# Kernel tuning notes

Measured on AMD Instinct MI355X. Metric: run time of the kernel, lower is better.

Reference implementation:

```python
import math
import jax
import jax.numpy as jnp
from jax import lax
import numpy as np

B, T, S, C, E = 16, 1024, 2048, 256, 256
STRIDE, MAX_SAMPLES, SIGMA, RAND_START = 20, 20, 3.0, 0


def setup_inputs():
    key = jax.random.key(0)
    ks = jax.random.split(key, 6)
    return {
        "x": jax.random.normal(ks[0], (B, T, C), jnp.float32),
        "target_embedding": jax.random.normal(ks[1], (B, T, E), jnp.float32),
        # scale keys so pre-softmax scores are O(1..10) like a trained model
        "enc_keys": jax.random.normal(ks[2], (B, E, S), jnp.float32) * 0.05,
        "enc_values": jax.random.normal(ks[3], (B, S, E), jnp.float32),
        "W_in": jax.random.normal(ks[4], (E, C), jnp.float32) * math.sqrt(1.0 / C),
        "b_in": jnp.zeros((E,), jnp.float32),
        "W_out": jax.random.normal(ks[5], (C, E), jnp.float32) * math.sqrt(1.0 / E),
        "b_out": jnp.zeros((C,), jnp.float32),
    }


def _get_matrix(attn, sim_vec, stride, start):
    # attn: [B,T,S], sim_vec: [B,S,E]
    nrm = sim_vec / jnp.linalg.norm(sim_vec, axis=2, keepdims=True)
    attn_avg = jnp.mean(attn, axis=1)[..., None]          # [B,S,1]
    ns = nrm[:, start::stride, :]                          # [B,N,E]
    aa = attn_avg[:, start::stride, :]                     # [B,N,1]
    sim = jnp.einsum('bne,bme->bnm', ns, ns)               # cosine similarity
    qual = aa @ jnp.swapaxes(aa, 1, 2)                     # quality outer product
    return qual * sim                                      # DPP kernel L [B,N,N]


def _bfgm(L, max_samples):
    # Vectorized faithful version of the greedy Cholesky DPP MAP loop.
    Bv, N, _ = L.shape
    bidx = jnp.arange(Bv)
    D0 = jnp.diagonal(L, axis1=1, axis2=2)                 # [B,N]
    mask0 = jnp.ones((Bv, N), L.dtype)
    J0 = jnp.argmax(jnp.log(D0 * mask0), axis=1)
    mask0 = mask0.at[bidx, J0].set(0.0)
    C0 = jnp.zeros((Bv, N, max_samples), L.dtype)          # col 0 stays zero (as in torch)

    def step(carry, t):
        Cm, D, J, mask = carry
        Lj = L[bidx, J, :]                                 # [B,N] = L[b, J[b], i]
        cj = Cm[bidx, J, :]                                # [B,K]
        cdot = jnp.einsum('bnk,bk->bn', Cm, cj)            # <c_i, c_j>
        dj = D[bidx, J][:, None]
        e = (Lj - cdot) / dj * mask                        # zero at already-selected
        Cm = Cm.at[:, :, t].set(e)
        D = D - e * e
        J = jnp.argmax(jnp.log(D * mask), axis=1)
        mask = mask.at[bidx, J].set(0.0)
        return (Cm, D, J, mask), J

    (_, _, _, _), Js = lax.scan(step, (C0, D0, J0, mask0), jnp.arange(1, max_samples))
    all_J = jnp.concatenate([J0[None, :], Js], axis=0).T   # [B,max_samples]
    return jnp.sort(all_J, axis=1)                         # = nonzero(1-mask) order


def _create_gm(mu, sigma, length):
    pos = jnp.arange(length, dtype=jnp.float32)            # [S]
    z = pos[None, None, :] - mu[:, :, None].astype(jnp.float32)
    g = jnp.exp(-(z * z) / (2.0 * sigma * sigma)) / (math.sqrt(2.0 * math.pi) * sigma)
    return jnp.sum(g, axis=1)                              # [B,S]


def _forward(x, target_embedding, enc_keys, enc_values, W_in, b_in, W_out, b_out):
    residual = x
    h = (jnp.einsum('btc,ec->bte', x, W_in) + b_in + target_embedding) * math.sqrt(0.5)
    scores = jnp.einsum('bte,bes->bts', h, enc_keys)       # [B,T,S]
    attn = jax.nn.softmax(scores, axis=-1)
    # DPP auxiliary KL loss (training path, encoder_padding_mask=None); the
    # kernel / greedy selection / target distribution carry no gradient.
    L = _get_matrix(lax.stop_gradient(attn), lax.stop_gradient(enc_values), STRIDE, RAND_START)
    mu = _bfgm(L, MAX_SAMPLES)
    dist = jax.nn.softmax(_create_gm(mu, SIGMA, scores.shape[2]), axis=1)
    x_mean = jnp.mean(attn, axis=1)                        # [B,S]
    kl = jnp.sum(x_mean * (jnp.log(x_mean) - dist))        # KLDivLoss(input=dist, target=x_mean, sum)
    out = jnp.einsum('bts,bse->bte', attn, enc_values)
    s = enc_values.shape[1]
    out = out * (s * math.sqrt(1.0 / s))                   # = sqrt(s)
    out = (jnp.einsum('bte,ce->btc', out, W_out) + b_out + residual) * math.sqrt(0.5)
    return out, attn, -kl


def reference(x, target_embedding, enc_keys, enc_values, W_in, b_in, W_out, b_out):
    return _forward(x, target_embedding, enc_keys, enc_values, W_in, b_in, W_out, b_out)
```

## Files before the change

kernel.cpp:

```cpp
#include <hip/hip_runtime.h>
#include <math.h>

#define BB 16
#define TT 1024
#define SS 2048
#define CC 256
#define EE 256
#define NSUB 103
#define MAXS 20
#define STRIDE_ 20
#define XCH 32

static constexpr float RSQRT2  = 0.70710678118654752440f;
static constexpr float SQRT_S  = 45.25483399593904f;
static constexpr float GNORM   = 0.13298076013381093f;
static constexpr float INV2S2  = 0.055555555555555555f;

typedef __attribute__((ext_vector_type(8))) __bf16 bf16x8;
typedef __attribute__((ext_vector_type(4))) float  f32x4;

__device__ __forceinline__ float wave_sum(float v) {
    #pragma unroll
    for (int o = 32; o; o >>= 1) v += __shfl_down(v, o);
    return v;
}
__device__ __forceinline__ float wave_max(float v) {
    #pragma unroll
    for (int o = 32; o; o >>= 1) v = fmaxf(v, __shfl_down(v, o));
    return v;
}
__device__ __forceinline__ unsigned short f2bf(float f) {
    unsigned int u = __float_as_uint(f);
    u = (u + 0x7FFFu + ((u >> 16) & 1u)) >> 16;
    return (unsigned short)u;
}
__device__ __forceinline__ float bf2f(unsigned short s) {
    return __uint_as_float(((unsigned int)s) << 16);
}

#define GLD_LDS16(g, l) __builtin_amdgcn_global_load_lds(                      \
    (const __attribute__((address_space(1))) void*)(g),                        \
    (__attribute__((address_space(3))) void*)(l), 16, 0, 0)

__global__ __launch_bounds__(256) void k_cast3(
    const float* __restrict__ a,  unsigned short* __restrict__ oa, int na,
    const float* __restrict__ b2, unsigned short* __restrict__ ob, int nb,
    const float* __restrict__ c2, unsigned short* __restrict__ oc, int nc)
{
    int i = blockIdx.x * 256 + threadIdx.x;
    const float* in; unsigned short* out;
    if (i < na)                { in = a;  out = oa; }
    else if (i < na + nb)      { in = b2; out = ob; i -= na; }
    else if (i < na + nb + nc) { in = c2; out = oc; i -= na + nb; }
    else return;
    const float4 v = reinterpret_cast<const float4*>(in)[i];
    union { unsigned short u[4]; unsigned long long v8; } pk;
    pk.u[0] = f2bf(v.x); pk.u[1] = f2bf(v.y);
    pk.u[2] = f2bf(v.z); pk.u[3] = f2bf(v.w);
    reinterpret_cast<unsigned long long*>(out)[i] = pk.v8;
}

__global__ __launch_bounds__(256) void k_transpose_bf16(
    const float* __restrict__ in, unsigned short* __restrict__ out, int R, int Cc)
{
    __shared__ float t[64][65];
    const int b = blockIdx.z;
    const int r0 = blockIdx.x * 64, c0 = blockIdx.y * 64;
    const float* ip = in + (size_t)b * R * Cc;
    unsigned short* op = out + (size_t)b * R * Cc;
    const int tx = threadIdx.x & 63, ty = threadIdx.x >> 6;
    #pragma unroll
    for (int i = 0; i < 16; ++i)
        t[ty + 4 * i][tx] = ip[(size_t)(r0 + ty + 4 * i) * Cc + c0 + tx];
    __syncthreads();
    #pragma unroll
    for (int i = 0; i < 16; ++i)
        op[(size_t)(c0 + ty + 4 * i) * R + r0 + tx] = f2bf(t[tx][ty + 4 * i]);
}

template<int BM, int BN, int MODE>
__global__ __launch_bounds__(256) void k_gemm(
    const unsigned short* __restrict__ Abase,
    const unsigned short* __restrict__ Btbase,
    const float* __restrict__ bias, const float* __restrict__ add,
    float* __restrict__ Obase, unsigned short* __restrict__ Obbase,
    int M, int Nn, int K, float scale)
{
    constexpr int BK = 64;
    constexpr int AR = BM / 32;
    constexpr int BR = BN / 32;
    constexpr int WM = BM / 2, WN = BN / 2;
    constexpr int MI = WM / 16, NJ = WN / 16;

    __shared__ unsigned short As[BM * BK];
    __shared__ unsigned short Bs[BN * BK];

    const int nwg = gridDim.x * gridDim.y * gridDim.z;
    int l = blockIdx.x + gridDim.x * (blockIdx.y + gridDim.y * blockIdx.z);
    if ((nwg & 7) == 0) l = (l & 7) * (nwg >> 3) + (l >> 3);
    const int bx = l % gridDim.x; l /= gridDim.x;
    const int by = l % gridDim.y;
    const int b  = l / gridDim.y;

    const int m0 = bx * BM;
    const int n0 = by * BN;
    const unsigned short* A  = Abase  + (size_t)b * M  * K;
    const unsigned short* Bt = Btbase + (size_t)b * Nn * K;

    const int tid  = threadIdx.x;
    const int w    = tid >> 6;
    const int lane = tid & 63;
    const int wm   = w & 1, wn = w >> 1;

    const int sr  = tid >> 3;
    const int skb = ((tid & 7) << 4) ^ ((sr & 7) << 4);
    const unsigned short* ga[AR];
    const unsigned short* gb[BR];
    #pragma unroll
    for (int p = 0; p < AR; ++p)
        ga[p] = A + (size_t)(m0 + p * 32 + sr) * K + (skb >> 1);
    #pragma unroll
    for (int p = 0; p < BR; ++p)
        gb[p] = Bt + (size_t)(n0 + p * 32 + sr) * K + (skb >> 1);

    const int fr = lane & 15;
    const int qb = (lane >> 4) << 4;

    f32x4 acc[MI][NJ];
    #pragma unroll
    for (int i = 0; i < MI; ++i)
        #pragma unroll
        for (int j = 0; j < NJ; ++j)
            acc[i][j] = (f32x4){0.f, 0.f, 0.f, 0.f};

    for (int k0 = 0; k0 < K; k0 += BK) {
        #pragma unroll
        for (int p = 0; p < AR; ++p) GLD_LDS16(ga[p], As + p * 2048 + w * 512);
        #pragma unroll
        for (int p = 0; p < BR; ++p) GLD_LDS16(gb[p], Bs + p * 2048 + w * 512);
        #pragma unroll
        for (int p = 0; p < AR; ++p) ga[p] += BK;
        #pragma unroll
        for (int p = 0; p < BR; ++p) gb[p] += BK;
        __syncthreads();
        #pragma unroll
        for (int c = 0; c < 2; ++c) {
            bf16x8 af[MI], bf[NJ];
            #pragma unroll
            for (int i = 0; i < MI; ++i) {
                const int row = wm * WM + i * 16 + fr;
                const int byt = row * 128 + ((c * 64 + qb) ^ ((row & 7) << 4));
                af[i] = *reinterpret_cast<const bf16x8*>(
                            reinterpret_cast<const char*>(As) + byt);
            }
            #pragma unroll
            for (int j = 0; j < NJ; ++j) {
                const int row = wn * WN + j * 16 + fr;
                const int byt = row * 128 + ((c * 64 + qb) ^ ((row & 7) << 4));
                bf[j] = *reinterpret_cast<const bf16x8*>(
                            reinterpret_cast<const char*>(Bs) + byt);
            }
            #pragma unroll
            for (int i = 0; i < MI; ++i)
                #pragma unroll
                for (int j = 0; j < NJ; ++j)
                    acc[i][j] = __builtin_amdgcn_mfma_f32_16x16x32_bf16(af[i], bf[j], acc[i][j], 0, 0, 0);
        }
        __syncthreads();
    }

    float* Of = (MODE == 0 || MODE == 1) ? Obase + (size_t)b * M * Nn : nullptr;
    unsigned short* Ob = (MODE == 2 || MODE == 3) ? Obbase + (size_t)b * M * Nn : nullptr;
    const int rb = (lane >> 4) * 4;
    #pragma unroll
    for (int i = 0; i < MI; ++i)
        #pragma unroll
        for (int j = 0; j < NJ; ++j) {
            const int n = n0 + wn * WN + j * 16 + fr;
            #pragma unroll
            for (int r2 = 0; r2 < 4; ++r2) {
                const int m = m0 + wm * WM + i * 16 + rb + r2;
                const size_t idx = (size_t)m * Nn + n;
                if (MODE == 0) {
                    Of[idx] = acc[i][j][r2] * scale;
                } else if (MODE == 1) {
                    Of[idx] = (acc[i][j][r2] + bias[n] + add[idx]) * RSQRT2;
                } else if (MODE == 2) {
                    Ob[idx] = f2bf((acc[i][j][r2] + bias[n] + add[idx]) * RSQRT2);
                } else {
                    Ob[idx] = f2bf(acc[i][j][r2] * scale);
                }
            }
        }
}

__global__ __launch_bounds__(256) void k_softmax(float* __restrict__ attn,
                                                 unsigned short* __restrict__ attnb)
{
    float* p = attn + (size_t)blockIdx.x * SS;
    unsigned short* pb = attnb + (size_t)blockIdx.x * SS;
    const int tid = threadIdx.x;
    __shared__ float w[4];
    union { unsigned short u[8]; uint4 v4; } in;
    in.v4 = *reinterpret_cast<const uint4*>(&pb[tid * 8]);
    float v[8];
    #pragma unroll
    for (int i = 0; i < 8; ++i) v[i] = bf2f(in.u[i]);
    float mx = -INFINITY;
    #pragma unroll
    for (int i = 0; i < 8; ++i) mx = fmaxf(mx, v[i]);
    float wm = wave_max(mx);
    if ((tid & 63) == 0) w[tid >> 6] = wm;
    __syncthreads();
    const float m = fmaxf(fmaxf(w[0], w[1]), fmaxf(w[2], w[3]));
    float s = 0.f;
    #pragma unroll
    for (int i = 0; i < 8; ++i) { v[i] = expf(v[i] - m); s += v[i]; }
    __syncthreads();
    float wsv = wave_sum(s);
    if ((tid & 63) == 0) w[tid >> 6] = wsv;
    __syncthreads();
    const float inv = 1.0f / (w[0] + w[1] + w[2] + w[3]);
    float4 o0, o1;
    o0.x = v[0] * inv; o0.y = v[1] * inv; o0.z = v[2] * inv; o0.w = v[3] * inv;
    o1.x = v[4] * inv; o1.y = v[5] * inv; o1.z = v[6] * inv; o1.w = v[7] * inv;
    *reinterpret_cast<float4*>(&p[tid * 8])     = o0;
    *reinterpret_cast<float4*>(&p[tid * 8 + 4]) = o1;
    union { unsigned short u[8]; uint4 v4; } pk;
    pk.u[0] = f2bf(o0.x); pk.u[1] = f2bf(o0.y); pk.u[2] = f2bf(o0.z); pk.u[3] = f2bf(o0.w);
    pk.u[4] = f2bf(o1.x); pk.u[5] = f2bf(o1.y); pk.u[6] = f2bf(o1.z); pk.u[7] = f2bf(o1.w);
    *reinterpret_cast<uint4*>(&pb[tid * 8]) = pk.v4;
}

__global__ __launch_bounds__(256) void k_xmean_part(const unsigned short* __restrict__ attnb,
                                                    float* __restrict__ part)
{
    const int c = blockIdx.x, b = blockIdx.y;
    const unsigned short* p = attnb + ((size_t)b * TT + (size_t)c * (TT / XCH)) * SS
                              + threadIdx.x * 8;
    float acc[8] = {0.f, 0.f, 0.f, 0.f, 0.f, 0.f, 0.f, 0.f};
    #pragma unroll 8
    for (int t = 0; t < TT / XCH; ++t) {
        union { unsigned short u[8]; uint4 v4; } ld;
        ld.v4 = *reinterpret_cast<const uint4*>(p + (size_t)t * SS);
        #pragma unroll
        for (int i = 0; i < 8; ++i) acc[i] += bf2f(ld.u[i]);
    }
    float* o = part + ((size_t)b * XCH + c) * SS + threadIdx.x * 8;
    #pragma unroll
    for (int i = 0; i < 8; ++i) o[i] = acc[i];
}

__global__ __launch_bounds__(256) void k_ns(const float* __restrict__ ev,
                                            const float* __restrict__ part,
                                            float* __restrict__ ns, float* __restrict__ aa,
                                            float* __restrict__ klp)
{
    const int n = blockIdx.x, b = blockIdx.y;
    const int tid = threadIdx.x;
    if (n == 0 && b == 0 && tid == 0) klp[0] = 0.0f;
    const float* rowp = ev + ((size_t)b * SS + (size_t)n * STRIDE_) * EE;
    const float v = rowp[tid];
    __shared__ float w[4];
    float r = wave_sum(v * v);
    if ((tid & 63) == 0) w[tid >> 6] = r;
    float pv = (tid < XCH) ? part[((size_t)b * XCH + tid) * SS + n * STRIDE_] : 0.f;
    float psum = wave_sum(pv);
    __syncthreads();
    const float nrm = sqrtf(w[0] + w[1] + w[2] + w[3]);
    ns[((size_t)b * NSUB + n) * EE + tid] = v / nrm;
    if (tid == 0) aa[b * NSUB + n] = psum * (1.0f / TT);
}

__global__ __launch_bounds__(128) void k_L(const float* __restrict__ ns,
                                           const float* __restrict__ aa,
                                           float* __restrict__ Lm)
{
    const int i = blockIdx.x, b = blockIdx.y;
    const int tid = threadIdx.x;
    __shared__ float nsi[EE];
    nsi[tid]       = ns[((size_t)b * NSUB + i) * EE + tid];
    nsi[tid + 128] = ns[((size_t)b * NSUB + i) * EE + tid + 128];
    __syncthreads();
    const float ai = aa[b * NSUB + i];
    for (int j = tid; j < NSUB; j += 128) {
        const float* rj = ns + ((size_t)b * NSUB + j) * EE;
        float d = 0.f;
        #pragma unroll 4
        for (int e = 0; e < EE; ++e) d += nsi[e] * rj[e];
        Lm[((size_t)b * NSUB + i) * NSUB + j] = d * ai * aa[b * NSUB + j];
    }
}

__global__ __launch_bounds__(256) void k_bfgm_kl(const float* __restrict__ Lm,
                                                 const float* __restrict__ part,
                                                 float* __restrict__ outkl)
{
    const int b = blockIdx.x;
    const int tid = threadIdx.x;
    const float* L = Lm + (size_t)b * NSUB * NSUB;
    __shared__ float D[128], mask[128], Cm[128 * MAXS], cj[MAXS], musS[MAXS];
    __shared__ float rv[4];
    __shared__ int   ri[4];
    __shared__ int   Jsh;
    __shared__ float w[4];
    const bool half = tid < 128;
    const bool act  = tid < NSUB;
    if (half) {
        D[tid]    = act ? L[(size_t)tid * NSUB + tid] : 0.0f;
        mask[tid] = act ? 1.0f : 0.0f;
        #pragma unroll
        for (int k = 0; k < MAXS; ++k) Cm[tid * MAXS + k] = 0.0f;
    }
    __syncthreads();

    auto argmax_step = [&](int t) {
        float key = act ? logf(D[tid] * mask[tid]) : -INFINITY;
        if (isnan(key)) key = INFINITY;
        float v = key; int idx = tid;
        #pragma unroll
        for (int o = 32; o; o >>= 1) {
            float ov = __shfl_down(v, o); int oi = __shfl_down(idx, o);
            if (ov > v || (ov == v && oi < idx)) { v = ov; idx = oi; }
        }
        if ((tid & 63) == 0) { rv[tid >> 6] = v; ri[tid >> 6] = idx; }
        __syncthreads();
        if (tid == 0) {
            float bv = rv[0]; int bi = ri[0];
            #pragma unroll
            for (int q2 = 1; q2 < 4; ++q2)
                if (rv[q2] > bv || (rv[q2] == bv && ri[q2] < bi)) { bv = rv[q2]; bi = ri[q2]; }
            Jsh = bi; mask[bi] = 0.0f; musS[t] = (float)bi;
        }
        __syncthreads();
    };

    argmax_step(0);
    for (int t = 1; t < MAXS; ++t) {
        if (tid < MAXS) cj[tid] = Cm[Jsh * MAXS + tid];
        __syncthreads();
        const int J = Jsh;
        const float dj = D[J];
        float e = 0.0f;
        if (act) {
            const float Ljn = L[(size_t)J * NSUB + tid];
            float cd = 0.f;
            #pragma unroll
            for (int k = 0; k < MAXS; ++k) cd += Cm[tid * MAXS + k] * cj[k];
            e = (Ljn - cd) / dj * mask[tid];
        }
        if (half) { Cm[tid * MAXS + t] = e; D[tid] -= e * e; }
        __syncthreads();
        argmax_step(t);
    }

    float xm[8];
    #pragma unroll
    for (int i = 0; i < 8; ++i) {
        float s = 0.f;
        #pragma unroll 8
        for (int c2 = 0; c2 < XCH; ++c2)
            s += part[((size_t)b * XCH + c2) * SS + tid + (i << 8)];
        xm[i] = s * (1.0f / TT);
    }
    float g[8];
    float mx = -INFINITY;
    #pragma unroll
    for (int i = 0; i < 8; ++i) {
        const float s = (float)(tid + (i << 8));
        float acc = 0.f;
        #pragma unroll
        for (int m = 0; m < MAXS; ++m) { const float z = s - musS[m]; acc += expf(-(z * z) * INV2S2); }
        g[i] = acc * GNORM;
        mx = fmaxf(mx, g[i]);
    }
    float wm = wave_max(mx);
    if ((tid & 63) == 0) w[tid >> 6] = wm;
    __syncthreads();
    const float m = fmaxf(fmaxf(w[0], w[1]), fmaxf(w[2], w[3]));
    float sum = 0.f;
    #pragma unroll
    for (int i = 0; i < 8; ++i) { g[i] = expf(g[i] - m); sum += g[i]; }
    __syncthreads();
    float wsv = wave_sum(sum);
    if ((tid & 63) == 0) w[tid >> 6] = wsv;
    __syncthreads();
    const float inv = 1.0f / (w[0] + w[1] + w[2] + w[3]);
    float acc2 = 0.f;
    #pragma unroll
    for (int i = 0; i < 8; ++i)
        acc2 += xm[i] * (logf(xm[i]) - g[i] * inv);
    __syncthreads();
    float wp = wave_sum(acc2);
    if ((tid & 63) == 0) w[tid >> 6] = wp;
    __syncthreads();
    if (tid == 0) atomicAdd(outkl, -(w[0] + w[1] + w[2] + w[3]));
}

extern "C" void kernel_launch(void* const* d_in, const int* in_sizes, int n_in,
                              void* d_out, int out_size, void* d_ws, size_t ws_size,
                              hipStream_t stream)
{
    const float* x     = (const float*)d_in[0];
    const float* te    = (const float*)d_in[1];
    const float* keys  = (const float*)d_in[2];
    const float* vals  = (const float*)d_in[3];
    const float* W_in  = (const float*)d_in[4];
    const float* b_in  = (const float*)d_in[5];
    const float* W_out = (const float*)d_in[6];
    const float* b_out = (const float*)d_in[7];

    float* outp = (float*)d_out;
    float* attn = outp + (size_t)BB * TT * CC;
    float* klp  = attn + (size_t)BB * TT * SS;

    unsigned short* X       = (unsigned short*)d_ws;
    unsigned short* x_bf    = X;
    unsigned short* Win_bf  = x_bf   + (size_t)BB * TT * CC;
    unsigned short* Wout_bf = Win_bf + (size_t)EE * CC;
    unsigned short* h_bf    = Wout_bf+ (size_t)CC * EE;
    unsigned short* keysT   = h_bf   + (size_t)BB * TT * EE;
    unsigned short* valsT   = keysT  + (size_t)BB * SS * EE;
    unsigned short* attnb   = valsT  + (size_t)BB * EE * SS;
    unsigned short* mid_bf  = attnb  + (size_t)BB * TT * SS;
    float* fws   = (float*)(mid_bf + (size_t)BB * TT * EE + 8);
    float* part  = fws;
    float* ns    = part  + (size_t)BB * XCH * SS;
    float* aa    = ns    + (size_t)BB * NSUB * EE;
    float* Lm    = aa    + (size_t)BB * NSUB;

    {
        const int na = BB * TT * CC / 4, nb = EE * CC / 4, nc = CC * EE / 4;
        const int blocks = (na + nb + nc + 255) / 256;
        k_cast3<<<blocks, 256, 0, stream>>>(x, x_bf, na, W_in, Win_bf, nb, W_out, Wout_bf, nc);
    }
    k_gemm<64, 64, 2><<<dim3(256, 4, 1), 256, 0, stream>>>(
        x_bf, Win_bf, b_in, te, nullptr, h_bf, BB * TT, CC, CC, 1.0f);
    k_transpose_bf16<<<dim3(4, 32, BB), 256, 0, stream>>>(keys, keysT, EE, SS);
    k_gemm<128, 128, 3><<<dim3(8, 16, BB), 256, 0, stream>>>(
        h_bf, keysT, nullptr, nullptr, nullptr, attnb, TT, SS, EE, 1.0f);
    k_transpose_bf16<<<dim3(32, 4, BB), 256, 0, stream>>>(vals, valsT, SS, EE);
    k_softmax<<<BB * TT, 256, 0, stream>>>(attn, attnb);
    k_xmean_part<<<dim3(XCH, BB), 256, 0, stream>>>(attnb, part);
    k_ns<<<dim3(NSUB, BB), 256, 0, stream>>>(vals, part, ns, aa, klp);
    k_L<<<dim3(NSUB, BB), 128, 0, stream>>>(ns, aa, Lm);
    k_bfgm_kl<<<BB, 256, 0, stream>>>(Lm, part, klp);
    k_gemm<64, 128, 3><<<dim3(16, 2, BB), 256, 0, stream>>>(
        attnb, valsT, nullptr, nullptr, nullptr, mid_bf, TT, EE, SS, SQRT_S);
    k_gemm<64, 64, 1><<<dim3(256, 4, 1), 256, 0, stream>>>(
        mid_bf, Wout_bf, b_out, x, outp, nullptr, BB * TT, CC, CC, 1.0f);
}
```

Baseline: 460.4 us.

## Fuse QK^T score GEMM with row softmax in a single kernel

Replaces the separate score GEMM (which wrote bf16 scores) and softmax kernel with one kernel. Each 512-thread block computes a full 32x2048 score tile in MFMA registers, reduces the row max and sum across waves through shared memory, and writes fp32 and bf16 probabilities directly. This removes the bf16 score round trip through global memory and one launch. In exchange it reads the keys straight from global memory without LDS staging, holds large register accumulators that limit occupancy, and uses scattered scalar stores. The BFGM shared Cm array also gets padded to stride 21 to avoid LDS bank conflicts.

```diff
diff --git a/kernel.cpp b/kernel.cpp
--- a/kernel.cpp
+++ b/kernel.cpp
@@ -194,42 +194,171 @@
         }
 }
 
-__global__ __launch_bounds__(256) void k_softmax(float* __restrict__ attn,
-                                                 unsigned short* __restrict__ attnb)
-{
-    float* p = attn + (size_t)blockIdx.x * SS;
-    unsigned short* pb = attnb + (size_t)blockIdx.x * SS;
-    const int tid = threadIdx.x;
-    __shared__ float w[4];
-    union { unsigned short u[8]; uint4 v4; } in;
-    in.v4 = *reinterpret_cast<const uint4*>(&pb[tid * 8]);
-    float v[8];
-    #pragma unroll
-    for (int i = 0; i < 8; ++i) v[i] = bf2f(in.u[i]);
-    float mx = -INFINITY;
-    #pragma unroll
-    for (int i = 0; i < 8; ++i) mx = fmaxf(mx, v[i]);
-    float wm = wave_max(mx);
-    if ((tid & 63) == 0) w[tid >> 6] = wm;
-    __syncthreads();
-    const float m = fmaxf(fmaxf(w[0], w[1]), fmaxf(w[2], w[3]));
-    float s = 0.f;
-    #pragma unroll
-    for (int i = 0; i < 8; ++i) { v[i] = expf(v[i] - m); s += v[i]; }
-    __syncthreads();
-    float wsv = wave_sum(s);
-    if ((tid & 63) == 0) w[tid >> 6] = wsv;
-    __syncthreads();
-    const float inv = 1.0f / (w[0] + w[1] + w[2] + w[3]);
-    float4 o0, o1;
-    o0.x = v[0] * inv; o0.y = v[1] * inv; o0.z = v[2] * inv; o0.w = v[3] * inv;
-    o1.x = v[4] * inv; o1.y = v[5] * inv; o1.z = v[6] * inv; o1.w = v[7] * inv;
-    *reinterpret_cast<float4*>(&p[tid * 8])     = o0;
-    *reinterpret_cast<float4*>(&p[tid * 8 + 4]) = o1;
-    union { unsigned short u[8]; uint4 v4; } pk;
-    pk.u[0] = f2bf(o0.x); pk.u[1] = f2bf(o0.y); pk.u[2] = f2bf(o0.z); pk.u[3] = f2bf(o0.w);
-    pk.u[4] = f2bf(o1.x); pk.u[5] = f2bf(o1.y); pk.u[6] = f2bf(o1.z); pk.u[7] = f2bf(o1.w);
-    *reinterpret_cast<uint4*>(&pb[tid * 8]) = pk.v4;
+__global__ __launch_bounds__(512) void k_qk_softmax(
+    const unsigned short* __restrict__ h,
+    const unsigned short* __restrict__ keysT,
+    float* __restrict__ attn,
+    unsigned short* __restrict__ attnb)
+{
+    __shared__ unsigned short hs[32 * 256];
+    __shared__ float red[8 * 32];
+    __shared__ float rowred[32];
+
+    int l = blockIdx.x + gridDim.x * blockIdx.y;
+    l = (l & 7) * 64 + (l >> 3);
+    const int tb = l & 31;
+    const int b  = l >> 5;
+
+    const int tid = threadIdx.x, w = tid >> 6, lane = tid & 63;
+    const int fr = lane & 15;
+    const int q8 = (lane >> 4) * 8;
+    const int qb = q8 * 2;
+
+    {
+        const int sr = tid >> 5;
+        const int cb = (tid & 31) << 4;
+        #pragma unroll
+        for (int p = 0; p < 2; ++p) {
+            const int row = p * 16 + sr;
+            const int scb = cb ^ ((row & 7) << 4);
+            const unsigned short* g =
+                h + ((size_t)b * TT + tb * 32 + row) * EE + (scb >> 1);
+            GLD_LDS16(g, hs + p * 4096 + w * 512);
+        }
+    }
+    __syncthreads();
+
+    const int n0w = w * 256;
+    const unsigned short* Kb = keysT + (size_t)b * SS * EE;
+
+    f32x4 acc[2][16];
+    #pragma unroll
+    for (int i = 0; i < 2; ++i)
+        #pragma unroll
+        for (int j = 0; j < 16; ++j)
+            acc[i][j] = (f32x4){0.f, 0.f, 0.f, 0.f};
+
+    #pragma unroll
+    for (int kk = 0; kk < 8; ++kk) {
+        bf16x8 af[2];
+        #pragma unroll
+        for (int i = 0; i < 2; ++i) {
+            const int row = i * 16 + fr;
+            const int byt = row * 512 + ((kk * 64 + qb) ^ ((row & 7) << 4));
+            af[i] = *reinterpret_cast<const bf16x8*>(
+                        reinterpret_cast<const char*>(hs) + byt);
+        }
+        #pragma unroll
+        for (int c = 0; c < 4; ++c) {
+            #pragma unroll
+            for (int j2 = 0; j2 < 4; ++j2) {
+                const int n = n0w + c * 64 + j2 * 16 + fr;
+                const bf16x8 bf = *reinterpret_cast<const bf16x8*>(
+                                      Kb + (size_t)n * EE + kk * 32 + q8);
+                acc[0][c * 4 + j2] = __builtin_amdgcn_mfma_f32_16x16x32_bf16(
+                    af[0], bf, acc[0][c * 4 + j2], 0, 0, 0);
+                acc[1][c * 4 + j2] = __builtin_amdgcn_mfma_f32_16x16x32_bf16(
+                    af[1], bf, acc[1][c * 4 + j2], 0, 0, 0);
+            }
+        }
+    }
+
+    const int rb = (lane >> 4) * 4;
+
+    float mxr[2][4];
+    #pragma unroll
+    for (int i = 0; i < 2; ++i)
+        #pragma unroll
+        for (int r2 = 0; r2 < 4; ++r2) {
+            float m = acc[i][0][r2];
+            #pragma unroll
+            for (int j = 1; j < 16; ++j) m = fmaxf(m, acc[i][j][r2]);
+            mxr[i][r2] = m;
+        }
+    #pragma unroll
+    for (int o = 1; o < 16; o <<= 1)
+        #pragma unroll
+        for (int i = 0; i < 2; ++i)
+            #pragma unroll
+            for (int r2 = 0; r2 < 4; ++r2)
+                mxr[i][r2] = fmaxf(mxr[i][r2], __shfl_xor(mxr[i][r2], o));
+    if (fr == 0) {
+        #pragma unroll
+        for (int i = 0; i < 2; ++i)
+            #pragma unroll
+            for (int r2 = 0; r2 < 4; ++r2)
+                red[w * 32 + i * 16 + rb + r2] = mxr[i][r2];
+    }
+    __syncthreads();
+    if (tid < 32) {
+        float m = red[tid];
+        #pragma unroll
+        for (int ww = 1; ww < 8; ++ww) m = fmaxf(m, red[ww * 32 + tid]);
+        rowred[tid] = m;
+    }
+    __syncthreads();
+    float mfin[2][4];
+    #pragma unroll
+    for (int i = 0; i < 2; ++i)
+        #pragma unroll
+        for (int r2 = 0; r2 < 4; ++r2)
+            mfin[i][r2] = rowred[i * 16 + rb + r2];
+    __syncthreads();
+
+    float sm[2][4] = {{0.f, 0.f, 0.f, 0.f}, {0.f, 0.f, 0.f, 0.f}};
+    #pragma unroll
+    for (int i = 0; i < 2; ++i)
+        #pragma unroll
+        for (int j = 0; j < 16; ++j)
+            #pragma unroll
+            for (int r2 = 0; r2 < 4; ++r2) {
+                const float p = expf(acc[i][j][r2] - mfin[i][r2]);
+                acc[i][j][r2] = p;
+                sm[i][r2] += p;
+            }
+    #pragma unroll
+    for (int o = 1; o < 16; o <<= 1)
+        #pragma unroll
+        for (int i = 0; i < 2; ++i)
+            #pragma unroll
+            for (int r2 = 0; r2 < 4; ++r2)
+                sm[i][r2] += __shfl_xor(sm[i][r2], o);
+    if (fr == 0) {
+        #pragma unroll
+        for (int i = 0; i < 2; ++i)
+            #pragma unroll
+            for (int r2 = 0; r2 < 4; ++r2)
+                red[w * 32 + i * 16 + rb + r2] = sm[i][r2];
+    }
+    __syncthreads();
+    if (tid < 32) {
+        float s = red[tid];
+        #pragma unroll
+        for (int ww = 1; ww < 8; ++ww) s += red[ww * 32 + tid];
+        rowred[tid] = 1.0f / s;
+    }
+    __syncthreads();
+    float inv[2][4];
+    #pragma unroll
+    for (int i = 0; i < 2; ++i)
+        #pragma unroll
+        for (int r2 = 0; r2 < 4; ++r2)
+            inv[i][r2] = rowred[i * 16 + rb + r2];
+
+    const size_t tbase = (size_t)b * TT + (size_t)tb * 32;
+    #pragma unroll
+    for (int i = 0; i < 2; ++i)
+        #pragma unroll
+        for (int r2 = 0; r2 < 4; ++r2) {
+            const size_t rowoff = (tbase + i * 16 + rb + r2) * SS;
+            #pragma unroll
+            for (int j = 0; j < 16; ++j) {
+                const int col = n0w + (j >> 2) * 64 + (j & 3) * 16 + fr;
+                const float p = acc[i][j][r2] * inv[i][r2];
+                attn[rowoff + col]  = p;
+                attnb[rowoff + col] = f2bf(p);
+            }
+        }
 }
 
 __global__ __launch_bounds__(256) void k_xmean_part(const unsigned short* __restrict__ attnb,
@@ -299,7 +428,7 @@
     const int b = blockIdx.x;
     const int tid = threadIdx.x;
     const float* L = Lm + (size_t)b * NSUB * NSUB;
-    __shared__ float D[128], mask[128], Cm[128 * MAXS], cj[MAXS], musS[MAXS];
+    __shared__ float D[128], mask[128], Cm[128 * 21], cj[MAXS], musS[MAXS];
     __shared__ float rv[4];
     __shared__ int   ri[4];
     __shared__ int   Jsh;
@@ -310,7 +439,7 @@
         D[tid]    = act ? L[(size_t)tid * NSUB + tid] : 0.0f;
         mask[tid] = act ? 1.0f : 0.0f;
         #pragma unroll
-        for (int k = 0; k < MAXS; ++k) Cm[tid * MAXS + k] = 0.0f;
+        for (int k = 0; k < MAXS; ++k) Cm[tid * 21 + k] = 0.0f;
     }
     __syncthreads();
 
@@ -337,7 +466,7 @@
 
     argmax_step(0);
     for (int t = 1; t < MAXS; ++t) {
-        if (tid < MAXS) cj[tid] = Cm[Jsh * MAXS + tid];
+        if (tid < MAXS) cj[tid] = Cm[Jsh * 21 + tid];
         __syncthreads();
         const int J = Jsh;
         const float dj = D[J];
@@ -346,10 +475,10 @@
             const float Ljn = L[(size_t)J * NSUB + tid];
             float cd = 0.f;
             #pragma unroll
-            for (int k = 0; k < MAXS; ++k) cd += Cm[tid * MAXS + k] * cj[k];
+            for (int k = 0; k < MAXS; ++k) cd += Cm[tid * 21 + k] * cj[k];
             e = (Ljn - cd) / dj * mask[tid];
         }
-        if (half) { Cm[tid * MAXS + t] = e; D[tid] -= e * e; }
+        if (half) { Cm[tid * 21 + t] = e; D[tid] -= e * e; }
         __syncthreads();
         argmax_step(t);
     }
@@ -437,10 +566,8 @@
     k_gemm<64, 64, 2><<<dim3(256, 4, 1), 256, 0, stream>>>(
         x_bf, Win_bf, b_in, te, nullptr, h_bf, BB * TT, CC, CC, 1.0f);
     k_transpose_bf16<<<dim3(4, 32, BB), 256, 0, stream>>>(keys, keysT, EE, SS);
-    k_gemm<128, 128, 3><<<dim3(8, 16, BB), 256, 0, stream>>>(
-        h_bf, keysT, nullptr, nullptr, nullptr, attnb, TT, SS, EE, 1.0f);
+    k_qk_softmax<<<dim3(TT / 32, BB), 512, 0, stream>>>(h_bf, keysT, attn, attnb);
     k_transpose_bf16<<<dim3(32, 4, BB), 256, 0, stream>>>(vals, valsT, SS, EE);
-    k_softmax<<<BB * TT, 256, 0, stream>>>(attn, attnb);
     k_xmean_part<<<dim3(XCH, BB), 256, 0, stream>>>(attnb, part);
     k_ns<<<dim3(NSUB, BB), 256, 0, stream>>>(vals, part, ns, aa, klp);
     k_L<<<dim3(NSUB, BB), 128, 0, stream>>>(ns, aa, Lm);
```

Result: slower. 491.8 us (+6.8%).
